# Optimization experiments

Measured on AMD Instinct MI355X. Metric: run time of the kernel, lower is better.

Reference implementation:

```python
import jax, jax.numpy as jnp
import numpy as np

B, S, H, NH = 2, 2048, 2048, 32
HD = H // NH  # 64

def _causal_mask(b, s, dtype=jnp.float32):
    neg = jnp.finfo(dtype).min
    m = jnp.where(jnp.tril(jnp.ones((s, s), dtype=bool)), 0.0, neg).astype(dtype)
    return jnp.broadcast_to(m[None, None], (b, 1, s, s))

def setup_inputs() -> dict:
    key = jax.random.key(0)
    k1, k2, k3, k4, k5 = jax.random.split(key, 5)
    scale = 1.0 / np.sqrt(H)
    return {
        "hidden_states": jax.random.normal(k1, (B, S, H), jnp.float32),
        "attention_mask": _causal_mask(B, S),
        "Wq": jax.random.normal(k2, (H, H), jnp.float32) * scale,
        "Wk": jax.random.normal(k3, (H, H), jnp.float32) * scale,
        "Wv": jax.random.normal(k4, (H, H), jnp.float32) * scale,
        "Wo": jax.random.normal(k5, (H, H), jnp.float32) * scale,
    }

def reference(hidden_states, attention_mask, Wq, Wk, Wv, Wo):
    b, s, _ = hidden_states.shape
    dt = hidden_states.dtype
    def proj(W):  # torch Linear: x @ W.T -> [b, nh, s, hd]
        return (hidden_states @ W.T).reshape(b, s, NH, HD).transpose(0, 2, 1, 3)
    q, k, v = proj(Wq), proj(Wk), proj(Wv)
    attn = jnp.einsum('bhqd,bhkd->bhqk', q, k) / np.sqrt(HD)
    attn = attn + attention_mask
    attn = jnp.maximum(attn, jnp.finfo(attn.dtype).min)
    attn = jax.nn.softmax(attn.astype(jnp.float32), axis=-1).astype(dt)
    out = jnp.einsum('bhqk,bhkd->bhqd', attn, v)
    out = out.transpose(0, 2, 1, 3).reshape(b, s, H)
    return out @ Wo.T
```

## Files before the change

### kernel.cpp

```cpp
#include <hip/hip_runtime.h>
#include <hip/hip_bf16.h>
#include <stdint.h>

#define S_LEN 2048
#define NHEAD 32
#define HDIM  64

using bf16x8 = __attribute__((ext_vector_type(8))) short;
using f32x4  = __attribute__((ext_vector_type(4))) float;
using f32x16 = __attribute__((ext_vector_type(16))) float;

__device__ __forceinline__ uint16_t f2bf(float f) {
  union { float f; uint32_t u; } c; c.f = f;
  uint32_t u = c.u;
  return (uint16_t)((u + 0x7FFFu + ((u >> 16) & 1u)) >> 16);
}

__device__ __forceinline__ void load_lds16(const void* g, void* l) {
  __builtin_amdgcn_global_load_lds(
      (const __attribute__((address_space(1))) void*)g,
      (__attribute__((address_space(3))) void*)l, 16, 0, 0);
}

__device__ __forceinline__ f32x16 mfma32(bf16x8 a, bf16x8 b, f32x16 c) {
  return __builtin_amdgcn_mfma_f32_32x32x16_bf16(a, b, c, 0, 0, 0);
}

__device__ __forceinline__ uint32_t cvtpk(float lo, float hi_) {
  uint32_t d;
  asm("v_cvt_pk_bf16_f32 %0, %1, %2" : "=v"(d) : "v"(lo), "v"(hi_));
  return d;
}
__device__ __forceinline__ void plswap(uint32_t& a, uint32_t& b) {
  asm volatile("v_permlane32_swap_b32 %0, %1" : "+v"(a), "+v"(b));
}

__global__ __launch_bounds__(256) void conv_batch(
    const float* __restrict__ X, const float* __restrict__ Wq,
    const float* __restrict__ Wk, const float* __restrict__ Wv,
    uint16_t* __restrict__ Xbf, uint16_t* __restrict__ Wqk,
    uint16_t* __restrict__ Wvb) {
  int i = blockIdx.x * 256 + threadIdx.x;
  const float* src; uint16_t* dst; int o;
  if (i < 2097152)      { src = X;  dst = Xbf;           o = i; }
  else if (i < 3145728) { src = Wq; dst = Wqk;           o = i - 2097152; }
  else if (i < 4194304) { src = Wk; dst = Wqk + 4194304; o = i - 3145728; }
  else                  { src = Wv; dst = Wvb;           o = i - 4194304; }
  float4 v = ((const float4*)src)[o];
  uint64_t packed = (uint64_t)f2bf(v.x) | ((uint64_t)f2bf(v.y) << 16) |
                    ((uint64_t)f2bf(v.z) << 32) | ((uint64_t)f2bf(v.w) << 48);
  ((uint64_t*)dst)[o] = packed;
}

__global__ __launch_bounds__(256) void conv_f32_bf16(
    const float* __restrict__ in, uint16_t* __restrict__ out, int n4) {
  int i = blockIdx.x * 256 + threadIdx.x;
  if (i < n4) {
    float4 v = ((const float4*)in)[i];
    uint64_t packed = (uint64_t)f2bf(v.x) | ((uint64_t)f2bf(v.y) << 16) |
                      ((uint64_t)f2bf(v.z) << 32) | ((uint64_t)f2bf(v.w) << 48);
    ((uint64_t*)out)[i] = packed;
  }
}

__global__ __launch_bounds__(512, 2) void gemm_qk(
    const uint16_t* __restrict__ A, const uint16_t* __restrict__ Bw,
    uint16_t* __restrict__ Qo, uint16_t* __restrict__ Ko, float qscale) {
  extern __shared__ char smem[];
  const int t = threadIdx.x;
  const int lane = t & 63, w = t >> 6;
  const int lrow = lane & 15, lgrp = lane >> 4;
  const int wr = w >> 2, wc = w & 3;
  const int id = blockIdx.x;
  const int swz = (id & 7) * 32 + (id >> 3);
  const int bm = (swz & 15) * 256, bn = (swz >> 4) * 256;
  constexpr int NT = 2048 / 32;

  const f32x4 zero4 = {0.f, 0.f, 0.f, 0.f};
  f32x4 acc[8][4];
#pragma unroll
  for (int mi = 0; mi < 8; ++mi)
#pragma unroll
    for (int ni = 0; ni < 4; ++ni) acc[mi][ni] = zero4;

  auto stage_mat = [&](const uint16_t* __restrict__ G, int grow0,
                       char* ldsbase, int kt) {
#pragma unroll
    for (int j = 0; j < 2; ++j) {
      const int s = t + j * 512;
      const int row = s >> 2;
      const int sc = (s & 3) ^ ((row >> 1) & 3);
      load_lds16(G + (size_t)(grow0 + row) * 2048 + kt + sc * 8,
                 ldsbase + j * 8192 + w * 1024);
    }
  };
  auto lda = [&](const char* Ab, int mi) -> bf16x8 {
    const int row = wr * 128 + mi * 16 + lrow;
    return *(const bf16x8*)(Ab + row * 64 + ((lgrp ^ ((row >> 1) & 3)) << 4));
  };
  auto ldb = [&](const char* Bb, int ni) -> bf16x8 {
    const int row = wc * 64 + ni * 16 + lrow;
    return *(const bf16x8*)(Bb + row * 64 + ((lgrp ^ ((row >> 1) & 3)) << 4));
  };

  stage_mat(A, bm, smem, 0);
  stage_mat(Bw, bn, smem + 16384, 0);
  stage_mat(A, bm, smem + 32768, 32);
  stage_mat(Bw, bn, smem + 32768 + 16384, 32);
  asm volatile("s_waitcnt vmcnt(4)" ::: "memory");
  __builtin_amdgcn_s_barrier();

  for (int kt = 0; kt < NT; ++kt) {
    char* cur = smem + (kt % 3) * 32768;
    char* nx2 = smem + ((kt + 2) % 3) * 32768;
    const int kg = (kt + 2) * 32;
    bf16x8 aF[4], bF[4];

    if (kt + 2 < NT) stage_mat(A, bm, nx2, kg);
#pragma unroll
    for (int mi = 0; mi < 4; ++mi) aF[mi] = lda(cur, mi);
#pragma unroll
    for (int ni = 0; ni < 4; ++ni) bF[ni] = ldb(cur + 16384, ni);
    __builtin_amdgcn_s_barrier();
    asm volatile("s_waitcnt lgkmcnt(0)" ::: "memory");
    __builtin_amdgcn_sched_barrier(0);
    __builtin_amdgcn_s_setprio(1);
#pragma unroll
    for (int mi = 0; mi < 4; ++mi)
#pragma unroll
      for (int ni = 0; ni < 4; ++ni)
        acc[mi][ni] = __builtin_amdgcn_mfma_f32_16x16x32_bf16(
            aF[mi], bF[ni], acc[mi][ni], 0, 0, 0);
    __builtin_amdgcn_s_setprio(0);
    __builtin_amdgcn_s_barrier();

    if (kt + 2 < NT) stage_mat(Bw, bn, nx2 + 16384, kg);
#pragma unroll
    for (int mi = 0; mi < 4; ++mi) aF[mi] = lda(cur, 4 + mi);
    __builtin_amdgcn_s_barrier();
    asm volatile("s_waitcnt lgkmcnt(0)" ::: "memory");
    __builtin_amdgcn_sched_barrier(0);
    __builtin_amdgcn_s_setprio(1);
#pragma unroll
    for (int mi = 0; mi < 4; ++mi)
#pragma unroll
      for (int ni = 0; ni < 4; ++ni)
        acc[4 + mi][ni] = __builtin_amdgcn_mfma_f32_16x16x32_bf16(
            aF[mi], bF[ni], acc[4 + mi][ni], 0, 0, 0);
    __builtin_amdgcn_s_setprio(0);
    if (kt < NT - 2) {
      asm volatile("s_waitcnt vmcnt(4)" ::: "memory");
    } else {
      asm volatile("s_waitcnt vmcnt(0)" ::: "memory");
    }
    __builtin_amdgcn_s_barrier();
  }

  const bool isQ = (bn < 2048);
#pragma unroll
  for (int mi = 0; mi < 8; ++mi) {
#pragma unroll
    for (int ni = 0; ni < 4; ++ni) {
      const int n = bn + wc * 64 + ni * 16 + lrow;
      const int n2 = isQ ? n : (n - 2048);
      const int h = n2 >> 6, d = n2 & 63;
#pragma unroll
      for (int r = 0; r < 4; ++r) {
        const int m = bm + wr * 128 + mi * 16 + lgrp * 4 + r;
        const int b = m >> 11, s = m & 2047;
        const size_t off = (((size_t)(b * NHEAD + h) * S_LEN + s) * HDIM) + d;
        if (isQ) Qo[off] = f2bf(acc[mi][ni][r] * qscale);
        else     Ko[off] = f2bf(acc[mi][ni][r]);
      }
    }
  }
}

template<int MODE>
__global__ __launch_bounds__(256) void gemm_nt(
    const uint16_t* __restrict__ A, const uint16_t* __restrict__ B,
    void* __restrict__ C, int M, int N, int K, float scale) {
  constexpr int BK = 64;
  __shared__ __align__(16) uint16_t As[128 * BK];
  __shared__ __align__(16) uint16_t Bs[128 * BK];

  const int t = threadIdx.x;
  const int lane = t & 63, w = t >> 6;
  const int lrow = lane & 15, lgrp = lane >> 4;
  const int bm = blockIdx.y * 128, bn = blockIdx.x * 128;
  const int wm = (w >> 1) * 64, wn = (w & 1) * 64;

  const f32x4 zero4 = {0.f, 0.f, 0.f, 0.f};
  f32x4 acc[4][4];
#pragma unroll
  for (int mi = 0; mi < 4; ++mi)
#pragma unroll
    for (int ni = 0; ni < 4; ++ni) acc[mi][ni] = zero4;

  const int rowS = t >> 3;
  const int chunk = t & 7;
  const int srcChunk = chunk ^ (rowS & 7);

  for (int kt = 0; kt < K; kt += BK) {
    __syncthreads();
#pragma unroll
    for (int it = 0; it < 4; ++it) {
      const int r = it * 32 + rowS;
      load_lds16(A + (size_t)(bm + r) * K + kt + srcChunk * 8,
                 (char*)As + it * 4096 + w * 1024);
      load_lds16(B + (size_t)(bn + r) * K + kt + srcChunk * 8,
                 (char*)Bs + it * 4096 + w * 1024);
    }
    __syncthreads();

#pragma unroll
    for (int ks = 0; ks < 2; ++ks) {
      bf16x8 af[4], bf[4];
#pragma unroll
      for (int mi = 0; mi < 4; ++mi) {
        const int ra = wm + mi * 16 + lrow;
        const int cb = ks * 4 + lgrp;
        af[mi] = *(const bf16x8*)((const char*)As +
                                  ra * 128 + ((cb ^ (ra & 7)) * 16));
        const int rb = wn + mi * 16 + lrow;
        bf[mi] = *(const bf16x8*)((const char*)Bs +
                                  rb * 128 + ((cb ^ (rb & 7)) * 16));
      }
#pragma unroll
      for (int mi = 0; mi < 4; ++mi)
#pragma unroll
        for (int ni = 0; ni < 4; ++ni)
          acc[mi][ni] = __builtin_amdgcn_mfma_f32_16x16x32_bf16(
              af[mi], bf[ni], acc[mi][ni], 0, 0, 0);
    }
  }

#pragma unroll
  for (int mi = 0; mi < 4; ++mi) {
#pragma unroll
    for (int ni = 0; ni < 4; ++ni) {
      const int n = bn + wn + ni * 16 + lrow;
#pragma unroll
      for (int r = 0; r < 4; ++r) {
        const int m = bm + wm + mi * 16 + lgrp * 4 + r;
        const float v = acc[mi][ni][r] * scale;
        if (MODE == 2) {
          ((float*)C)[(size_t)m * N + n] = v;
        } else {
          const int h = m >> 6, d = m & 63;
          const int b = n >> 11, s = n & 2047;
          ((uint16_t*)C)[(((size_t)(b * NHEAD + h) * HDIM + d) * S_LEN) + s] =
              f2bf(v);
        }
      }
    }
  }
}

__global__ __launch_bounds__(256, 3) void attn_kernel(
    const uint16_t* __restrict__ Q, const uint16_t* __restrict__ K,
    const uint16_t* __restrict__ Vt, uint16_t* __restrict__ O) {
  __shared__ __align__(16) uint16_t Ks[2][64 * 64];
  __shared__ __align__(16) uint16_t Vs[2][64 * 64];
  __shared__ float Ls[4][32];

  const int t = threadIdx.x, lane = t & 63, w = t >> 6;
  const int qcol = lane & 31, hi = lane >> 5;
  const int id = blockIdx.x;
  const int bh = (id & 7) * 8 + ((id >> 3) & 7);
  const int p = id >> 6;
  const int b = bh >> 5, h = bh & 31;

  const uint16_t* Qbh = Q + (size_t)bh * S_LEN * HDIM;
  const uint16_t* Kbh = K + (size_t)bh * S_LEN * HDIM;
  const uint16_t* Vbh = Vt + (size_t)bh * HDIM * S_LEN;

  const int srow = lane >> 3;
  const int schunk = (lane & 7) ^ srow;

  auto stage = [&](int k0, int bi) {
#pragma unroll
    for (int j = 0; j < 2; ++j) {
      const int r = j * 32 + w * 8 + srow;
      load_lds16(Kbh + (size_t)(k0 + r) * HDIM + schunk * 8,
                 (char*)&Ks[bi][0] + j * 4096 + w * 1024);
      load_lds16(Vbh + (size_t)r * S_LEN + k0 + schunk * 8,
                 (char*)&Vs[bi][0] + j * 4096 + w * 1024);
    }
  };

  for (int pass = 0; pass < 2; ++pass) {
    const int jq = pass ? (15 - p) : p;
    const int qw = jq * 128 + w * 32;
    const int qg = qw + qcol;

    bf16x8 qB[4];
    {
      const uint16_t* qp = Qbh + (size_t)(qw + qcol) * HDIM + hi * 8;
#pragma unroll
      for (int j = 0; j < 4; ++j) qB[j] = *(const bf16x8*)(qp + 16 * j);
    }

    f32x16 oacc0, oacc1;
#pragma unroll
    for (int r = 0; r < 16; ++r) { oacc0[r] = 0.f; oacc1[r] = 0.f; }
    float lsum = 0.f;

    const int nt = 2 * jq + 2;
    for (int kt = 0; kt < nt; ++kt) {
      const int cur = kt & 1;
      const int k0 = kt * 64;
      if (kt == 0) { __syncthreads(); stage(0, 0); }
      __syncthreads();
      if (kt + 1 < nt) stage((kt + 1) * 64, cur ^ 1);

      if (k0 <= qw + 31) {
        const char* Kc = (const char*)&Ks[cur][0];
        const char* Vc = (const char*)&Vs[cur][0];

        f32x16 s0, s1;
#pragma unroll
        for (int r = 0; r < 16; ++r) { s0[r] = 0.f; s1[r] = 0.f; }
        const int rk0 = qcol, rk1 = 32 + qcol;
        const int x0 = rk0 & 7;
        __builtin_amdgcn_s_setprio(1);
#pragma unroll
        for (int j = 0; j < 4; ++j) {
          bf16x8 kf0 = *(const bf16x8*)(Kc + rk0 * 128 + (((2*j+hi) ^ x0) << 4));
          bf16x8 kf1 = *(const bf16x8*)(Kc + rk1 * 128 + (((2*j+hi) ^ x0) << 4));
          s0 = mfma32(kf0, qB[j], s0);
          s1 = mfma32(kf1, qB[j], s1);
        }
        __builtin_amdgcn_s_setprio(0);

        if (k0 + 63 > qw) {
#pragma unroll
          for (int r = 0; r < 16; ++r) {
            const int krow = (r & 3) + 8 * (r >> 2) + 4 * hi;
            s0[r] = (k0 + krow <= qg) ? __expf(s0[r]) : 0.f;
            s1[r] = (k0 + 32 + krow <= qg) ? __expf(s1[r]) : 0.f;
            lsum += s0[r] + s1[r];
          }
        } else {
#pragma unroll
          for (int r = 0; r < 16; ++r) {
            s0[r] = __expf(s0[r]);
            s1[r] = __expf(s1[r]);
            lsum += s0[r] + s1[r];
          }
        }

        bf16x8 paf[4];
#pragma unroll
        for (int tt = 0; tt < 4; ++tt) {
          const int o = 8 * (tt & 1);
          uint32_t a0, a1, a2, a3;
          if (tt < 2) {
            a0 = cvtpk(s0[o + 0], s0[o + 1]);
            a1 = cvtpk(s0[o + 2], s0[o + 3]);
            a2 = cvtpk(s0[o + 4], s0[o + 5]);
            a3 = cvtpk(s0[o + 6], s0[o + 7]);
          } else {
            a0 = cvtpk(s1[o + 0], s1[o + 1]);
            a1 = cvtpk(s1[o + 2], s1[o + 3]);
            a2 = cvtpk(s1[o + 4], s1[o + 5]);
            a3 = cvtpk(s1[o + 6], s1[o + 7]);
          }
          plswap(a0, a2);
          plswap(a1, a3);
          union { uint32_t u[4]; bf16x8 v; } pk;
          pk.u[0] = a0; pk.u[1] = a1; pk.u[2] = a2; pk.u[3] = a3;
          paf[tt] = pk.v;
        }

        __builtin_amdgcn_s_setprio(1);
#pragma unroll
        for (int tt = 0; tt < 4; ++tt) {
          const int c = 2 * tt + hi;
          bf16x8 v0f = *(const bf16x8*)(Vc + rk0 * 128 + ((c ^ x0) << 4));
          bf16x8 v1f = *(const bf16x8*)(Vc + rk1 * 128 + ((c ^ x0) << 4));
          oacc0 = mfma32(paf[tt], v0f, oacc0);
          oacc1 = mfma32(paf[tt], v1f, oacc1);
        }
        __builtin_amdgcn_s_setprio(0);
      }
    }

    lsum += __shfl_xor(lsum, 32, 64);
    if (hi == 0) Ls[w][qcol] = 1.0f / lsum;

#pragma unroll
    for (int r = 0; r < 16; ++r) {
      const int qrow = (r & 3) + 8 * (r >> 2) + 4 * hi;
      const float inv = Ls[w][qrow];
      const size_t base = ((size_t)b * S_LEN + qw + qrow) * 2048 + h * 64;
      O[base + qcol] = f2bf(oacc0[r] * inv);
      O[base + 32 + qcol] = f2bf(oacc1[r] * inv);
    }
  }
}

extern "C" void kernel_launch(void* const* d_in, const int* in_sizes, int n_in,
                              void* d_out, int out_size, void* d_ws,
                              size_t ws_size, hipStream_t stream) {
  const float* X  = (const float*)d_in[0];
  const float* Wq = (const float*)d_in[2];
  const float* Wk = (const float*)d_in[3];
  const float* Wv = (const float*)d_in[4];
  const float* Wo = (const float*)d_in[5];
  float* out = (float*)d_out;

  char* ws = (char*)d_ws;
  uint16_t* Xbf = (uint16_t*)ws;
  uint16_t* Wqk = (uint16_t*)(ws + 16777216);
  uint16_t* Qb  = (uint16_t*)(ws + 33554432);
  uint16_t* Kb  = (uint16_t*)(ws + 50331648);
  uint16_t* Wsm = (uint16_t*)(ws + 67108864);
  uint16_t* Vtb = Wqk;
  uint16_t* Ob  = Xbf;

  const float qscale = 0.125f;

  hipFuncSetAttribute((const void*)gemm_qk,
                      hipFuncAttributeMaxDynamicSharedMemorySize, 98304);

  conv_batch<<<20480, 256, 0, stream>>>(X, Wq, Wk, Wv, Xbf, Wqk, Wsm);
  gemm_qk<<<256, 512, 98304, stream>>>(Xbf, Wqk, Qb, Kb, qscale);
  gemm_nt<1><<<dim3(32, 16), 256, 0, stream>>>(Wsm, Xbf, Vtb, 2048, 4096, 2048, 1.0f);
  attn_kernel<<<dim3(512), 256, 0, stream>>>(Qb, Kb, Vtb, Ob);
  conv_f32_bf16<<<4096, 256, 0, stream>>>(Wo, Wsm, 1048576);
  gemm_nt<2><<<dim3(16, 32), 256, 0, stream>>>(Ob, Wsm, out, 4096, 2048, 2048, 1.0f);
}
```

Before: 234.2 us.

## Simplify QK projection pipeline and add triple-buffered async loads to gemm_nt

The QK projection kernel's two-half interleaved stage/compute loop is replaced with a simpler triple-buffered loop. Each iteration now waits, syncs once, issues both A and B prefetches for two tiles ahead, and runs all 32 MFMAs, with no setprio or sched barriers. The generic gemm_nt drops its synchronous double __syncthreads BK=64 loop in favour of a 3-stage async global-to-LDS pipeline with BK=32 and launch_bounds occupancy 3. The intent is to overlap global loads with MFMA work in gemm_nt, at the cost of losing the finer-grained interleaving and priority hints in the QK kernel.

```diff
diff --git a/kernel.cpp b/kernel.cpp
--- a/kernel.cpp
+++ b/kernel.cpp
@@ -107,53 +107,30 @@
   stage_mat(Bw, bn, smem + 16384, 0);
   stage_mat(A, bm, smem + 32768, 32);
   stage_mat(Bw, bn, smem + 32768 + 16384, 32);
-  asm volatile("s_waitcnt vmcnt(4)" ::: "memory");
-  __builtin_amdgcn_s_barrier();
 
   for (int kt = 0; kt < NT; ++kt) {
     char* cur = smem + (kt % 3) * 32768;
-    char* nx2 = smem + ((kt + 2) % 3) * 32768;
-    const int kg = (kt + 2) * 32;
-    bf16x8 aF[4], bF[4];
-
-    if (kt + 2 < NT) stage_mat(A, bm, nx2, kg);
-#pragma unroll
-    for (int mi = 0; mi < 4; ++mi) aF[mi] = lda(cur, mi);
+    if (kt < NT - 1) asm volatile("s_waitcnt vmcnt(4)" ::: "memory");
+    else             asm volatile("s_waitcnt vmcnt(0)" ::: "memory");
+    __builtin_amdgcn_s_barrier();
+
+    if (kt + 2 < NT) {
+      char* nx2 = smem + ((kt + 2) % 3) * 32768;
+      stage_mat(A, bm, nx2, (kt + 2) * 32);
+      stage_mat(Bw, bn, nx2 + 16384, (kt + 2) * 32);
+    }
+
+    bf16x8 aF[8], bF[4];
+#pragma unroll
+    for (int mi = 0; mi < 8; ++mi) aF[mi] = lda(cur, mi);
 #pragma unroll
     for (int ni = 0; ni < 4; ++ni) bF[ni] = ldb(cur + 16384, ni);
-    __builtin_amdgcn_s_barrier();
-    asm volatile("s_waitcnt lgkmcnt(0)" ::: "memory");
-    __builtin_amdgcn_sched_barrier(0);
-    __builtin_amdgcn_s_setprio(1);
-#pragma unroll
-    for (int mi = 0; mi < 4; ++mi)
+#pragma unroll
+    for (int mi = 0; mi < 8; ++mi)
 #pragma unroll
       for (int ni = 0; ni < 4; ++ni)
         acc[mi][ni] = __builtin_amdgcn_mfma_f32_16x16x32_bf16(
             aF[mi], bF[ni], acc[mi][ni], 0, 0, 0);
-    __builtin_amdgcn_s_setprio(0);
-    __builtin_amdgcn_s_barrier();
-
-    if (kt + 2 < NT) stage_mat(Bw, bn, nx2 + 16384, kg);
-#pragma unroll
-    for (int mi = 0; mi < 4; ++mi) aF[mi] = lda(cur, 4 + mi);
-    __builtin_amdgcn_s_barrier();
-    asm volatile("s_waitcnt lgkmcnt(0)" ::: "memory");
-    __builtin_amdgcn_sched_barrier(0);
-    __builtin_amdgcn_s_setprio(1);
-#pragma unroll
-    for (int mi = 0; mi < 4; ++mi)
-#pragma unroll
-      for (int ni = 0; ni < 4; ++ni)
-        acc[4 + mi][ni] = __builtin_amdgcn_mfma_f32_16x16x32_bf16(
-            aF[mi], bF[ni], acc[4 + mi][ni], 0, 0, 0);
-    __builtin_amdgcn_s_setprio(0);
-    if (kt < NT - 2) {
-      asm volatile("s_waitcnt vmcnt(4)" ::: "memory");
-    } else {
-      asm volatile("s_waitcnt vmcnt(0)" ::: "memory");
-    }
-    __builtin_amdgcn_s_barrier();
   }
 
   const bool isQ = (bn < 2048);
@@ -177,18 +154,17 @@
 }
 
 template<int MODE>
-__global__ __launch_bounds__(256) void gemm_nt(
+__global__ __launch_bounds__(256, 3) void gemm_nt(
     const uint16_t* __restrict__ A, const uint16_t* __restrict__ B,
     void* __restrict__ C, int M, int N, int K, float scale) {
-  constexpr int BK = 64;
-  __shared__ __align__(16) uint16_t As[128 * BK];
-  __shared__ __align__(16) uint16_t Bs[128 * BK];
+  __shared__ __align__(16) char smem[3][16384];
 
   const int t = threadIdx.x;
   const int lane = t & 63, w = t >> 6;
   const int lrow = lane & 15, lgrp = lane >> 4;
   const int bm = blockIdx.y * 128, bn = blockIdx.x * 128;
   const int wm = (w >> 1) * 64, wn = (w & 1) * 64;
+  const int NT = K / 32;
 
   const f32x4 zero4 = {0.f, 0.f, 0.f, 0.f};
   f32x4 acc[4][4];
@@ -197,42 +173,50 @@
 #pragma unroll
     for (int ni = 0; ni < 4; ++ni) acc[mi][ni] = zero4;
 
-  const int rowS = t >> 3;
-  const int chunk = t & 7;
-  const int srcChunk = chunk ^ (rowS & 7);
-
-  for (int kt = 0; kt < K; kt += BK) {
-    __syncthreads();
-#pragma unroll
-    for (int it = 0; it < 4; ++it) {
-      const int r = it * 32 + rowS;
-      load_lds16(A + (size_t)(bm + r) * K + kt + srcChunk * 8,
-                 (char*)As + it * 4096 + w * 1024);
-      load_lds16(B + (size_t)(bn + r) * K + kt + srcChunk * 8,
-                 (char*)Bs + it * 4096 + w * 1024);
-    }
-    __syncthreads();
-
-#pragma unroll
-    for (int ks = 0; ks < 2; ++ks) {
-      bf16x8 af[4], bf[4];
-#pragma unroll
-      for (int mi = 0; mi < 4; ++mi) {
-        const int ra = wm + mi * 16 + lrow;
-        const int cb = ks * 4 + lgrp;
-        af[mi] = *(const bf16x8*)((const char*)As +
-                                  ra * 128 + ((cb ^ (ra & 7)) * 16));
-        const int rb = wn + mi * 16 + lrow;
-        bf[mi] = *(const bf16x8*)((const char*)Bs +
-                                  rb * 128 + ((cb ^ (rb & 7)) * 16));
-      }
-#pragma unroll
-      for (int mi = 0; mi < 4; ++mi)
-#pragma unroll
-        for (int ni = 0; ni < 4; ++ni)
-          acc[mi][ni] = __builtin_amdgcn_mfma_f32_16x16x32_bf16(
-              af[mi], bf[ni], acc[mi][ni], 0, 0, 0);
-    }
+  auto stage_mat = [&](const uint16_t* __restrict__ G, int grow0,
+                       char* ldsbase, int kt) {
+#pragma unroll
+    for (int j = 0; j < 2; ++j) {
+      const int s = t + j * 256;
+      const int row = s >> 2;
+      const int sc = (s & 3) ^ ((row >> 1) & 3);
+      load_lds16(G + (size_t)(grow0 + row) * K + kt + sc * 8,
+                 ldsbase + j * 4096 + w * 1024);
+    }
+  };
+  auto ldf = [&](const char* Mb, int base, int i) -> bf16x8 {
+    const int row = base + i * 16 + lrow;
+    return *(const bf16x8*)(Mb + row * 64 + ((lgrp ^ ((row >> 1) & 3)) << 4));
+  };
+
+  stage_mat(A, bm, smem[0], 0);
+  stage_mat(B, bn, smem[0] + 8192, 0);
+  stage_mat(A, bm, smem[1], 32);
+  stage_mat(B, bn, smem[1] + 8192, 32);
+
+  for (int kt = 0; kt < NT; ++kt) {
+    char* cur = smem[kt % 3];
+    if (kt < NT - 1) asm volatile("s_waitcnt vmcnt(4)" ::: "memory");
+    else             asm volatile("s_waitcnt vmcnt(0)" ::: "memory");
+    __builtin_amdgcn_s_barrier();
+
+    if (kt + 2 < NT) {
+      char* nx2 = smem[(kt + 2) % 3];
+      stage_mat(A, bm, nx2, (kt + 2) * 32);
+      stage_mat(B, bn, nx2 + 8192, (kt + 2) * 32);
+    }
+
+    bf16x8 aF[4], bF[4];
+#pragma unroll
+    for (int mi = 0; mi < 4; ++mi) aF[mi] = ldf(cur, wm, mi);
+#pragma unroll
+    for (int ni = 0; ni < 4; ++ni) bF[ni] = ldf(cur + 8192, wn, ni);
+#pragma unroll
+    for (int mi = 0; mi < 4; ++mi)
+#pragma unroll
+      for (int ni = 0; ni < 4; ++ni)
+        acc[mi][ni] = __builtin_amdgcn_mfma_f32_16x16x32_bf16(
+            aF[mi], bF[ni], acc[mi][ni], 0, 0, 0);
   }
 
 #pragma unroll
```

New measurement: 233.5 us. Within noise of the previous version (-0.3%).
